# Optimization experiments

Measured on AMD Instinct MI355X. Metric: run time of the kernel, lower is better.

The kernel has to match this reference:

```python
import jax, jax.numpy as jnp
import numpy as np

B, T, C, H = 8, 512, 1024, 16
N = C // H
DW, DA, DG = 64, 64, 128  # LoRA dims for decay / icl-rate / gate at C=1024

def _ln(x, w, b, eps=1e-5):
    mu = x.mean(-1, keepdims=True)
    var = ((x - mu) ** 2).mean(-1, keepdims=True)
    return (x - mu) * jax.lax.rsqrt(var + eps) * w + b

def _gn_heads(x, w, b, eps=64e-5):
    # GroupNorm(H groups) over channel dim of (B,T,C)
    xh = x.reshape(x.shape[0], x.shape[1], H, N)
    mu = xh.mean(-1, keepdims=True)
    var = ((xh - mu) ** 2).mean(-1, keepdims=True)
    xh = (xh - mu) * jax.lax.rsqrt(var + eps)
    return xh.reshape(x.shape) * w + b

def _shift(x):
    # RWKV time_shift: ZeroPad2d((0,0,1,-1))
    return jnp.concatenate([jnp.zeros_like(x[:, :1]), x[:, :-1]], axis=1)

def _wkv7(r, w_log, k, v, a, b):
    # all (B,T,H,N); state S (B,H,N,N): S = S*diag(exp(-exp(w))) + (S@a)b^T + v k^T; out = S@r
    decay = jnp.exp(-jnp.exp(w_log))
    def step(state, inp):
        r_t, d_t, k_t, v_t, a_t, b_t = inp
        sa = jnp.einsum('bhij,bhj->bhi', state, a_t)
        state = (state * d_t[:, :, None, :]
                 + sa[..., None] * b_t[:, :, None, :]
                 + v_t[..., None] * k_t[:, :, None, :])
        return state, jnp.einsum('bhij,bhj->bhi', state, r_t)
    xs = tuple(jnp.moveaxis(t, 1, 0) for t in (r, decay, k, v, a, b))
    s0 = jnp.zeros((r.shape[0], H, N, N), r.dtype)
    _, out = jax.lax.scan(step, s0, xs)
    return jnp.moveaxis(out, 0, 1)

def reference(x, v_first, ln_pre_w, ln_pre_b, ln_attn_w, ln_attn_b, ln_ffn_w, ln_ffn_b,
              x_r, x_w, x_k, x_v, x_a, x_g, w0, w1, w2, a0, a1, a2, g1, g2,
              k_k, k_a, r_k, W_r, W_k, W_v, W_o, gn_w, gn_b,
              ffn_x_k, W_ffn1, W_ffn2):
    Bx, Tx = x.shape[0], x.shape[1]
    x = _ln(x, ln_pre_w, ln_pre_b)            # pre_norm (layer_idx==0)
    # --- time mixing (RWKV7Attention) ---
    xn = _ln(x, ln_attn_w, ln_attn_b)
    dx = _shift(xn) - xn
    xr = xn + dx * x_r; xw = xn + dx * x_w; xk = xn + dx * x_k
    xv = xn + dx * x_v; xa = xn + dx * x_a; xg = xn + dx * x_g
    r = xr @ W_r
    w_log = -jax.nn.softplus(-(w0 + jnp.tanh(xw @ w1) @ w2)) - 0.5
    k = xk @ W_k
    v = xv @ W_v
    v_first = v                               # layer 0 stores v
    a = jax.nn.sigmoid(a0 + (xa @ a1) @ a2)   # in-context learning rate
    g = jax.nn.sigmoid(xg @ g1) @ g2          # gate
    kk = (k * k_k).reshape(Bx, Tx, H, N)
    kk = kk / jnp.maximum(jnp.linalg.norm(kk, axis=-1, keepdims=True), 1e-12)
    k = k * (1.0 + (a - 1.0) * k_a)
    rh = r.reshape(Bx, Tx, H, N)
    kh = k.reshape(Bx, Tx, H, N)
    vh = v.reshape(Bx, Tx, H, N)
    ah = a.reshape(Bx, Tx, H, N)
    o = _wkv7(rh, w_log.reshape(Bx, Tx, H, N), kh, vh, -kk, kk * ah)
    o = _gn_heads(o.reshape(Bx, Tx, C), gn_w, gn_b)
    o = o + ((rh * kh * r_k).sum(-1, keepdims=True) * vh).reshape(Bx, Tx, C)
    x = x + (o * g) @ W_o                     # residual (dropout p=0)
    # --- channel mixing (RWKV7FeedForward) ---
    xf = _ln(x, ln_ffn_w, ln_ffn_b)
    kf = xf + (_shift(xf) - xf) * ffn_x_k
    x = x + jnp.square(jax.nn.relu(kf @ W_ffn1)) @ W_ffn2
    return x, v_first

def setup_inputs() -> dict:
    key = jax.random.key(0)
    ks = iter(jax.random.split(key, 40))
    def nrm(shape, s=0.02):
        return jax.random.normal(next(ks), shape, jnp.float32) * s
    f32 = jnp.float32
    d = {
        'x': jax.random.normal(next(ks), (B, T, C), f32),
        'v_first': jnp.zeros((B, T, C), f32),
        'ln_pre_w': jnp.ones((C,), f32), 'ln_pre_b': jnp.zeros((C,), f32),
        'ln_attn_w': jnp.ones((C,), f32), 'ln_attn_b': jnp.zeros((C,), f32),
        'ln_ffn_w': jnp.ones((C,), f32), 'ln_ffn_b': jnp.zeros((C,), f32),
        'x_r': nrm((C,), 0.1), 'x_w': nrm((C,), 0.1), 'x_k': nrm((C,), 0.1),
        'x_v': nrm((C,), 0.1), 'x_a': nrm((C,), 0.1), 'x_g': nrm((C,), 0.1),
        'w0': nrm((C,), 0.5), 'w1': nrm((C, DW)), 'w2': nrm((DW, C)),
        'a0': nrm((C,), 0.1), 'a1': nrm((C, DA)), 'a2': nrm((DA, C)),
        'g1': nrm((C, DG)), 'g2': nrm((DG, C)),
        'k_k': 0.85 * jnp.ones((C,), f32) + nrm((C,), 0.05),
        'k_a': jnp.ones((C,), f32),
        'r_k': nrm((H, N), 0.1),
        'W_r': nrm((C, C)), 'W_k': nrm((C, C)), 'W_v': nrm((C, C)), 'W_o': nrm((C, C)),
        'gn_w': jnp.ones((C,), f32), 'gn_b': jnp.zeros((C,), f32),
        'ffn_x_k': nrm((C,), 0.1),
        'W_ffn1': nrm((C, 4 * C)), 'W_ffn2': nrm((4 * C, C)),
    }
    return d
```

## Files before the change

### kernel.cpp

```cpp
#include <hip/hip_runtime.h>

#define Bb 8
#define Tt 512
#define Cc 1024
#define Hh 16
#define Nh 64
#define Mm 4096
#define BTC 4194304
#define DEV __device__ __forceinline__

typedef __attribute__((ext_vector_type(8))) short short8;
typedef __attribute__((ext_vector_type(4))) float f32x4;

DEV unsigned short f2bf(float f) {
  unsigned int u = __builtin_bit_cast(unsigned int, f);
  u += 0x7fffu + ((u >> 16) & 1u);
  return (unsigned short)(u >> 16);
}

template <int CTRL>
DEV float dppadd(float x) {
  int xi = __builtin_bit_cast(int, x);
  int yi = __builtin_amdgcn_update_dpp(0, xi, CTRL, 0xF, 0xF, true);
  return x + __builtin_bit_cast(float, yi);
}

struct TDesc { const float* in; unsigned short* out; int K, N, bstart, nbx; };
struct TPack { TDesc d[12]; };

__global__ __launch_bounds__(256) void kt_transpose_multi(TPack p) {
  __shared__ float tile[32][33];
  const int bid = blockIdx.x;
  int i = 0;
  #pragma unroll
  for (int j = 1; j < 12; ++j) if (bid >= p.d[j].bstart) i = j;
  const float* in = p.d[i].in;
  unsigned short* out = p.d[i].out;
  const int K = p.d[i].K, N = p.d[i].N;
  const int local = bid - p.d[i].bstart;
  const int byq = local / p.d[i].nbx;
  const int bx = (local - byq * p.d[i].nbx) * 32;
  const int by = byq * 32;
  int tx = threadIdx.x, ty = threadIdx.y;
  #pragma unroll
  for (int q = ty; q < 32; q += 8) {
    int kk = by + q, nn = bx + tx;
    tile[q][tx] = (kk < K && nn < N) ? in[(size_t)kk * N + nn] : 0.f;
  }
  __syncthreads();
  #pragma unroll
  for (int q = ty; q < 32; q += 8) {
    int nn = bx + q, kk = by + tx;
    if (nn < N && kk < K) out[(size_t)nn * K + kk] = f2bf(tile[tx][q]);
  }
}

DEV void row_stats(float v0, float v1, float v2, float v3, float* red,
                   float& mu, float& rs, float eps) {
  float s = v0 + v1 + v2 + v3;
  float q = v0 * v0 + v1 * v1 + v2 * v2 + v3 * v3;
  #pragma unroll
  for (int o = 32; o; o >>= 1) { s += __shfl_down(s, o); q += __shfl_down(q, o); }
  int w = threadIdx.x >> 6;
  __syncthreads();
  if ((threadIdx.x & 63) == 0) { red[w] = s; red[4 + w] = q; }
  __syncthreads();
  s = red[0] + red[1] + red[2] + red[3];
  q = red[4] + red[5] + red[6] + red[7];
  mu = s * (1.f / 1024.f);
  float var = q * (1.f / 1024.f) - mu * mu;
  rs = rsqrtf(var + eps);
}

__global__ __launch_bounds__(256) void k1_mix(
    const float* __restrict__ x,
    const float* __restrict__ lnpw, const float* __restrict__ lnpb,
    const float* __restrict__ lnaw, const float* __restrict__ lnab,
    const float* __restrict__ cr, const float* __restrict__ cw,
    const float* __restrict__ ck, const float* __restrict__ cv,
    const float* __restrict__ ca, const float* __restrict__ cg,
    float* __restrict__ xln,
    unsigned short* __restrict__ mR, unsigned short* __restrict__ mW,
    unsigned short* __restrict__ mK, unsigned short* __restrict__ mV,
    unsigned short* __restrict__ mA, unsigned short* __restrict__ mG) {
  __shared__ float red[8];
  const int row = blockIdx.x;
  const int t = row & (Tt - 1);
  const int tid = threadIdx.x;
  const int c = tid * 4;
  const size_t base = (size_t)row * Cc + c;
  float a0 = x[base], a1 = x[base + 1], a2 = x[base + 2], a3 = x[base + 3];
  float mu, rs;
  row_stats(a0, a1, a2, a3, red, mu, rs, 1e-5f);
  float pw0 = lnpw[c], pw1 = lnpw[c + 1], pw2 = lnpw[c + 2], pw3 = lnpw[c + 3];
  float pb0 = lnpb[c], pb1 = lnpb[c + 1], pb2 = lnpb[c + 2], pb3 = lnpb[c + 3];
  float l0 = (a0 - mu) * rs * pw0 + pb0, l1 = (a1 - mu) * rs * pw1 + pb1;
  float l2 = (a2 - mu) * rs * pw2 + pb2, l3 = (a3 - mu) * rs * pw3 + pb3;
  float4 st; st.x = l0; st.y = l1; st.z = l2; st.w = l3;
  *(float4*)(xln + base) = st;
  row_stats(l0, l1, l2, l3, red, mu, rs, 1e-5f);
  float aw0 = lnaw[c], aw1 = lnaw[c + 1], aw2 = lnaw[c + 2], aw3 = lnaw[c + 3];
  float ab0 = lnab[c], ab1 = lnab[c + 1], ab2 = lnab[c + 2], ab3 = lnab[c + 3];
  float n0 = (l0 - mu) * rs * aw0 + ab0, n1 = (l1 - mu) * rs * aw1 + ab1;
  float n2 = (l2 - mu) * rs * aw2 + ab2, n3 = (l3 - mu) * rs * aw3 + ab3;
  float p0 = 0.f, p1 = 0.f, p2 = 0.f, p3 = 0.f;
  if (t > 0) {
    const size_t pb_ = base - Cc;
    float q0 = x[pb_], q1 = x[pb_ + 1], q2 = x[pb_ + 2], q3 = x[pb_ + 3];
    row_stats(q0, q1, q2, q3, red, mu, rs, 1e-5f);
    float e0 = (q0 - mu) * rs * pw0 + pb0, e1 = (q1 - mu) * rs * pw1 + pb1;
    float e2 = (q2 - mu) * rs * pw2 + pb2, e3 = (q3 - mu) * rs * pw3 + pb3;
    row_stats(e0, e1, e2, e3, red, mu, rs, 1e-5f);
    p0 = (e0 - mu) * rs * aw0 + ab0; p1 = (e1 - mu) * rs * aw1 + ab1;
    p2 = (e2 - mu) * rs * aw2 + ab2; p3 = (e3 - mu) * rs * aw3 + ab3;
  }
  float d0 = p0 - n0, d1 = p1 - n1, d2 = p2 - n2, d3 = p3 - n3;
  #define EMIT(cf, dst) { \
    float f0 = cf[c], f1 = cf[c + 1], f2 = cf[c + 2], f3 = cf[c + 3]; \
    ushort4 u; u.x = f2bf(n0 + d0 * f0); u.y = f2bf(n1 + d1 * f1); \
    u.z = f2bf(n2 + d2 * f2); u.w = f2bf(n3 + d3 * f3); \
    *(ushort4*)(dst + base) = u; }
  EMIT(cr, mR) EMIT(cw, mW) EMIT(ck, mK) EMIT(cv, mV) EMIT(ca, mA) EMIT(cg, mG)
  #undef EMIT
}

DEV void gll16(const unsigned short* g, unsigned short* l) {
  __builtin_amdgcn_global_load_lds(
      (const __attribute__((address_space(1))) void*)g,
      (__attribute__((address_space(3))) void*)l, 16, 0, 0);
}

template <int MODE>
DEV void gemm_epi(float z, size_t oi, int col,
                  float* outF, unsigned short* outB,
                  const float* bias, const float* res, float* outF2) {
  if constexpr (MODE == 0) outF[oi] = z;
  else if constexpr (MODE == 1) outB[oi] = f2bf(z);
  else if constexpr (MODE == 2) outB[oi] = f2bf(tanhf(z));
  else if constexpr (MODE == 3) outB[oi] = f2bf(1.f / (1.f + expf(-z)));
  else if constexpr (MODE == 4) { float m = fmaxf(z, 0.f); outB[oi] = f2bf(m * m); }
  else if constexpr (MODE == 5) { z += bias[col]; outF[oi] = 1.f / (1.f + expf(-z)); }
  else if constexpr (MODE == 6) {
    z += bias[col];
    float sg = 1.f / (1.f + expf(-z));
    outF[oi] = expf(-0.6065306597126334f * sg);
  } else if constexpr (MODE == 7) { outF[oi] = z + res[oi]; }
  else { float v = z + res[oi]; outF[oi] = v; outF2[oi] = v; }
}

DEV void gemm_epi_rt(int mode, float z, size_t oi, int col,
                     float* outF, unsigned short* outB, const float* bias) {
  if (mode == 0) outF[oi] = z;
  else if (mode == 1) outB[oi] = f2bf(z);
  else if (mode == 2) outB[oi] = f2bf(tanhf(z));
  else if (mode == 3) outB[oi] = f2bf(1.f / (1.f + expf(-z)));
  else if (mode == 5) { z += bias[col]; outF[oi] = 1.f / (1.f + expf(-z)); }
  else { z += bias[col]; float sg = 1.f / (1.f + expf(-z));
         outF[oi] = expf(-0.6065306597126334f * sg); }
}

template <int MODE>
__global__ __launch_bounds__(256) void kg_gemm64(
    const unsigned short* __restrict__ A, const unsigned short* __restrict__ Bt,
    int M, int Nn, int K,
    float* __restrict__ outF, unsigned short* __restrict__ outB,
    const float* __restrict__ bias, const float* __restrict__ res,
    float* __restrict__ outF2) {
  __shared__ unsigned short lsA[128 * 32];
  __shared__ unsigned short lsB[64 * 32];
  const int tid = threadIdx.x;
  const int lane = tid & 63;
  const int wave = tid >> 6;
  const int wy = wave >> 1, wx = wave & 1;
  const int m0 = blockIdx.y * 128;
  const int n0 = blockIdx.x * 64;
  const int sl4 = lane >> 2;
  const int sc = (lane & 3) << 3;
  f32x4 acc[4][2];
  #pragma unroll
  for (int i = 0; i < 4; ++i)
    #pragma unroll
    for (int j = 0; j < 2; ++j) { f32x4 z = {0.f, 0.f, 0.f, 0.f}; acc[i][j] = z; }
  const int fr = lane & 15;
  const int fk = (lane >> 4) << 3;
  for (int k0 = 0; k0 < K; k0 += 32) {
    #pragma unroll
    for (int j = 0; j < 2; ++j) {
      const int rb = (wave + j * 4) * 16;
      gll16(A + (size_t)(m0 + rb + sl4) * K + k0 + sc, lsA + rb * 32);
    }
    {
      const int rb = wave * 16;
      int br = n0 + rb + sl4;
      br = br < Nn ? br : Nn - 1;
      gll16(Bt + (size_t)br * K + k0 + sc, lsB + rb * 32);
    }
    __syncthreads();
    short8 af[4], bf[2];
    #pragma unroll
    for (int mt = 0; mt < 4; ++mt)
      af[mt] = *(const short8*)(lsA + (wy * 64 + mt * 16 + fr) * 32 + fk);
    #pragma unroll
    for (int nt = 0; nt < 2; ++nt)
      bf[nt] = *(const short8*)(lsB + (wx * 32 + nt * 16 + fr) * 32 + fk);
    #pragma unroll
    for (int mt = 0; mt < 4; ++mt)
      #pragma unroll
      for (int nt = 0; nt < 2; ++nt)
        acc[mt][nt] = __builtin_amdgcn_mfma_f32_16x16x32_bf16(af[mt], bf[nt], acc[mt][nt], 0, 0, 0);
    __syncthreads();
  }
  const int rbase = (lane >> 4) << 2;
  const int cbase = lane & 15;
  #pragma unroll
  for (int mt = 0; mt < 4; ++mt)
    #pragma unroll
    for (int nt = 0; nt < 2; ++nt)
      #pragma unroll
      for (int rr = 0; rr < 4; ++rr) {
        int row = m0 + wy * 64 + mt * 16 + rbase + rr;
        int col = n0 + wx * 32 + nt * 16 + cbase;
        if (col < Nn)
          gemm_epi<MODE>(acc[mt][nt][rr], (size_t)row * Nn + col, col, outF, outB, bias, res, outF2);
      }
}

DEV void gemm_body_rt(const unsigned short* A, const unsigned short* Bt,
                      int Nn, int K,
                      float* outF, unsigned short* outB, const float* bias,
                      unsigned short* lsA, unsigned short* lsB,
                      int m0, int n0, int mode) {
  const int tid = threadIdx.x;
  const int lane = tid & 63;
  const int wave = tid >> 6;
  const int wy = wave >> 1, wx = wave & 1;
  const int sl4 = lane >> 2;
  const int sc = (lane & 3) << 3;
  f32x4 acc[4][2];
  #pragma unroll
  for (int i = 0; i < 4; ++i)
    #pragma unroll
    for (int j = 0; j < 2; ++j) { f32x4 z = {0.f, 0.f, 0.f, 0.f}; acc[i][j] = z; }
  const int fr = lane & 15;
  const int fk = (lane >> 4) << 3;
  for (int k0 = 0; k0 < K; k0 += 32) {
    #pragma unroll
    for (int j = 0; j < 2; ++j) {
      const int rb = (wave + j * 4) * 16;
      gll16(A + (size_t)(m0 + rb + sl4) * K + k0 + sc, lsA + rb * 32);
    }
    {
      const int rb = wave * 16;
      int br = n0 + rb + sl4;
      br = br < Nn ? br : Nn - 1;
      gll16(Bt + (size_t)br * K + k0 + sc, lsB + rb * 32);
    }
    __syncthreads();
    short8 af[4], bf[2];
    #pragma unroll
    for (int mt = 0; mt < 4; ++mt)
      af[mt] = *(const short8*)(lsA + (wy * 64 + mt * 16 + fr) * 32 + fk);
    #pragma unroll
    for (int nt = 0; nt < 2; ++nt)
      bf[nt] = *(const short8*)(lsB + (wx * 32 + nt * 16 + fr) * 32 + fk);
    #pragma unroll
    for (int mt = 0; mt < 4; ++mt)
      #pragma unroll
      for (int nt = 0; nt < 2; ++nt)
        acc[mt][nt] = __builtin_amdgcn_mfma_f32_16x16x32_bf16(af[mt], bf[nt], acc[mt][nt], 0, 0, 0);
    __syncthreads();
  }
  const int rbase = (lane >> 4) << 2;
  const int cbase = lane & 15;
  #pragma unroll
  for (int mt = 0; mt < 4; ++mt)
    #pragma unroll
    for (int nt = 0; nt < 2; ++nt)
      #pragma unroll
      for (int rr = 0; rr < 4; ++rr) {
        int row = m0 + wy * 64 + mt * 16 + rbase + rr;
        int col = n0 + wx * 32 + nt * 16 + cbase;
        if (col < Nn)
          gemm_epi_rt(mode, acc[mt][nt][rr], (size_t)row * Nn + col, col, outF, outB, bias);
      }
}

__global__ __launch_bounds__(256) void kg_lora1(
    const unsigned short* __restrict__ mW, const unsigned short* __restrict__ mA,
    const unsigned short* __restrict__ mG,
    const unsigned short* __restrict__ w1T, const unsigned short* __restrict__ a1T,
    const unsigned short* __restrict__ g1T,
    unsigned short* __restrict__ tmpw, unsigned short* __restrict__ tmpa,
    unsigned short* __restrict__ tmpg) {
  __shared__ unsigned short lsA[128 * 32];
  __shared__ unsigned short lsB[64 * 32];
  const int z = blockIdx.z;
  const unsigned short* A  = z == 0 ? mW : z == 1 ? mA : mG;
  const unsigned short* Bt = z == 0 ? w1T : z == 1 ? a1T : g1T;
  unsigned short* outB     = z == 0 ? tmpw : z == 1 ? tmpa : tmpg;
  const int Nn = z < 2 ? 64 : 128;
  const int n0 = z < 2 ? 0 : (z - 2) * 64;
  const int mode = z == 0 ? 2 : z == 1 ? 1 : 3;
  gemm_body_rt(A, Bt, Nn, 1024, nullptr, outB, nullptr, lsA, lsB,
               blockIdx.y * 128, n0, mode);
}

__global__ __launch_bounds__(256) void kg_lora2(
    const unsigned short* __restrict__ tmpw, const unsigned short* __restrict__ tmpa,
    const unsigned short* __restrict__ tmpg,
    const unsigned short* __restrict__ w2T, const unsigned short* __restrict__ a2T,
    const unsigned short* __restrict__ g2T,
    float* __restrict__ decay, float* __restrict__ aicl, float* __restrict__ gout,
    const float* __restrict__ w0v, const float* __restrict__ a0v) {
  __shared__ unsigned short lsA[128 * 32];
  __shared__ unsigned short lsB[64 * 32];
  const int z = blockIdx.z;
  const unsigned short* A  = z == 0 ? tmpw : z == 1 ? tmpa : tmpg;
  const unsigned short* Bt = z == 0 ? w2T : z == 1 ? a2T : g2T;
  float* outF              = z == 0 ? decay : z == 1 ? aicl : gout;
  const float* bias        = z == 0 ? w0v : z == 1 ? a0v : nullptr;
  const int K = z < 2 ? 64 : 128;
  const int mode = z == 0 ? 6 : z == 1 ? 5 : 0;
  gemm_body_rt(A, Bt, 1024, K, outF, nullptr, bias, lsA, lsB,
               blockIdx.y * 128, blockIdx.x * 64, mode);
}

template <int MODE>
__global__ __launch_bounds__(512, 1) void kg_gemm8p(
    const unsigned short* __restrict__ A, const unsigned short* __restrict__ Bt,
    int Nn, int Kstride, int Klen,
    float* __restrict__ outF, unsigned short* __restrict__ outB) {
  __shared__ unsigned short lds[3 * 24576];
  const int tid = threadIdx.x;
  const int lane = tid & 63;
  const int wave = tid >> 6;
  const int wm = wave >> 2, wn = wave & 3;
  const int m0 = blockIdx.y * 128;
  const int n0 = blockIdx.x * 256;
  const int kbase = blockIdx.z * Klen;
  const int ntile = Klen / 64;
  const int fr = lane & 15;
  const int fkb = (lane >> 4) << 4;

  int arow[2], acolb[2], brow[4], bcolb[4];
  #pragma unroll
  for (int i = 0; i < 2; ++i) {
    int off = i * 8192 + tid * 16;
    int r = off >> 7;
    arow[i] = r; acolb[i] = (off & 127) ^ ((r & 7) << 4);
  }
  #pragma unroll
  for (int i = 0; i < 4; ++i) {
    int off = i * 8192 + tid * 16;
    int r = off >> 7;
    brow[i] = r; bcolb[i] = (off & 127) ^ ((r & 7) << 4);
  }

  #define STAGE(t_) { \
    int tc = (t_) < ntile ? (t_) : ntile - 1; \
    unsigned short* lb_ = lds + ((t_) % 3) * 24576; \
    const int kk = kbase + tc * 64; \
    _Pragma("unroll") \
    for (int i = 0; i < 2; ++i) \
      gll16(A + (size_t)(m0 + arow[i]) * Kstride + kk + (acolb[i] >> 1), \
            lb_ + i * 4096 + wave * 512); \
    _Pragma("unroll") \
    for (int i = 0; i < 4; ++i) \
      gll16(Bt + (size_t)(n0 + brow[i]) * Kstride + kk + (bcolb[i] >> 1), \
            lb_ + 8192 + i * 4096 + wave * 512); \
  }

  f32x4 acc[4][4];
  #pragma unroll
  for (int i = 0; i < 4; ++i)
    #pragma unroll
    for (int j = 0; j < 4; ++j) { f32x4 z = {0.f, 0.f, 0.f, 0.f}; acc[i][j] = z; }

  STAGE(0)
  STAGE(1)
  asm volatile("s_waitcnt vmcnt(6)" ::: "memory");
  __syncthreads();

  for (int t = 0; t < ntile; ++t) {
    STAGE(t + 2)
    const unsigned short* lb = lds + (t % 3) * 24576;
    #pragma unroll
    for (int ks = 0; ks < 2; ++ks) {
      short8 af[4], bf[4];
      #pragma unroll
      for (int mt = 0; mt < 4; ++mt) {
        int r = wm * 64 + mt * 16 + fr;
        int byt = (ks * 64 + fkb) ^ ((r & 7) << 4);
        af[mt] = *(const short8*)(lb + r * 64 + (byt >> 1));
      }
      #pragma unroll
      for (int nt = 0; nt < 4; ++nt) {
        int r = wn * 64 + nt * 16 + fr;
        int byt = (ks * 64 + fkb) ^ ((r & 7) << 4);
        bf[nt] = *(const short8*)(lb + 8192 + r * 64 + (byt >> 1));
      }
      __builtin_amdgcn_s_setprio(1);
      #pragma unroll
      for (int mt = 0; mt < 4; ++mt)
        #pragma unroll
        for (int nt = 0; nt < 4; ++nt)
          acc[mt][nt] = __builtin_amdgcn_mfma_f32_16x16x32_bf16(af[mt], bf[nt], acc[mt][nt], 0, 0, 0);
      __builtin_amdgcn_s_setprio(0);
    }
    asm volatile("s_waitcnt vmcnt(6)" ::: "memory");
    __syncthreads();
  }
  #undef STAGE

  const int rbase = (lane >> 4) << 2;
  const int cbase = lane & 15;
  #pragma unroll
  for (int mt = 0; mt < 4; ++mt)
    #pragma unroll
    for (int nt = 0; nt < 4; ++nt)
      #pragma unroll
      for (int rr = 0; rr < 4; ++rr) {
        int row = m0 + wm * 64 + mt * 16 + rbase + rr;
        int col = n0 + wn * 64 + nt * 16 + cbase;
        size_t oi = (size_t)row * Nn + col;
        float z = acc[mt][nt][rr];
        if constexpr (MODE == 4) { float m = fmaxf(z, 0.f); outB[oi] = f2bf(m * m); }
        else atomicAdd(outF + oi, z);
      }
}

__global__ __launch_bounds__(512, 1) void kg_qkv8p(
    const unsigned short* __restrict__ A0, const unsigned short* __restrict__ A1,
    const unsigned short* __restrict__ A2,
    const unsigned short* __restrict__ B0, const unsigned short* __restrict__ B1,
    const unsigned short* __restrict__ B2,
    float* __restrict__ rbuf, float* __restrict__ kbuf, float* __restrict__ vout,
    const float* __restrict__ aicl,
    const float* __restrict__ kkc, const float* __restrict__ kac,
    float* __restrict__ awb, float* __restrict__ bwb) {
  __shared__ unsigned short lds[3 * 24576];
  const int z = blockIdx.z;
  const unsigned short* A  = z == 0 ? A0 : z == 1 ? A1 : A2;
  const unsigned short* Bt = z == 0 ? B0 : z == 1 ? B1 : B2;
  const int tid = threadIdx.x;
  const int lane = tid & 63;
  const int wave = tid >> 6;
  const int wm = wave >> 2, wn = wave & 3;
  const int m0 = blockIdx.y * 128;
  const int n0 = blockIdx.x * 256;
  const int ntile = 16;
  const int fr = lane & 15;
  const int fkb = (lane >> 4) << 4;

  int arow[2], acolb[2], brow[4], bcolb[4];
  #pragma unroll
  for (int i = 0; i < 2; ++i) {
    int off = i * 8192 + tid * 16;
    int r = off >> 7;
    arow[i] = r; acolb[i] = (off & 127) ^ ((r & 7) << 4);
  }
  #pragma unroll
  for (int i = 0; i < 4; ++i) {
    int off = i * 8192 + tid * 16;
    int r = off >> 7;
    brow[i] = r; bcolb[i] = (off & 127) ^ ((r & 7) << 4);
  }

  #define STAGE(t_) { \
    int tc = (t_) < ntile ? (t_) : ntile - 1; \
    unsigned short* lb_ = lds + ((t_) % 3) * 24576; \
    const int kk = tc * 64; \
    _Pragma("unroll") \
    for (int i = 0; i < 2; ++i) \
      gll16(A + (size_t)(m0 + arow[i]) * 1024 + kk + (acolb[i] >> 1), \
            lb_ + i * 4096 + wave * 512); \
    _Pragma("unroll") \
    for (int i = 0; i < 4; ++i) \
      gll16(Bt + (size_t)(n0 + brow[i]) * 1024 + kk + (bcolb[i] >> 1), \
            lb_ + 8192 + i * 4096 + wave * 512); \
  }

  f32x4 acc[4][4];
  #pragma unroll
  for (int i = 0; i < 4; ++i)
    #pragma unroll
    for (int j = 0; j < 4; ++j) { f32x4 zz = {0.f, 0.f, 0.f, 0.f}; acc[i][j] = zz; }

  STAGE(0)
  STAGE(1)
  asm volatile("s_waitcnt vmcnt(6)" ::: "memory");
  __syncthreads();

  for (int t = 0; t < ntile; ++t) {
    STAGE(t + 2)
    const unsigned short* lb = lds + (t % 3) * 24576;
    #pragma unroll
    for (int ks = 0; ks < 2; ++ks) {
      short8 af[4], bf[4];
      #pragma unroll
      for (int mt = 0; mt < 4; ++mt) {
        int r = wm * 64 + mt * 16 + fr;
        int byt = (ks * 64 + fkb) ^ ((r & 7) << 4);
        af[mt] = *(const short8*)(lb + r * 64 + (byt >> 1));
      }
      #pragma unroll
      for (int nt = 0; nt < 4; ++nt) {
        int r = wn * 64 + nt * 16 + fr;
        int byt = (ks * 64 + fkb) ^ ((r & 7) << 4);
        bf[nt] = *(const short8*)(lb + 8192 + r * 64 + (byt >> 1));
      }
      __builtin_amdgcn_s_setprio(1);
      #pragma unroll
      for (int mt = 0; mt < 4; ++mt)
        #pragma unroll
        for (int nt = 0; nt < 4; ++nt)
          acc[mt][nt] = __builtin_amdgcn_mfma_f32_16x16x32_bf16(af[mt], bf[nt], acc[mt][nt], 0, 0, 0);
      __builtin_amdgcn_s_setprio(0);
    }
    asm volatile("s_waitcnt vmcnt(6)" ::: "memory");
    __syncthreads();
  }
  #undef STAGE

  const int rbase = (lane >> 4) << 2;
  const int cbase = lane & 15;
  if (z != 1) {
    float* outF = z == 0 ? rbuf : vout;
    #pragma unroll
    for (int mt = 0; mt < 4; ++mt)
      #pragma unroll
      for (int nt = 0; nt < 4; ++nt)
        #pragma unroll
        for (int rr = 0; rr < 4; ++rr) {
          int row = m0 + wm * 64 + mt * 16 + rbase + rr;
          int col = n0 + wn * 64 + nt * 16 + cbase;
          outF[(size_t)row * Cc + col] = acc[mt][nt][rr];
        }
  } else {
    float kkc4[4], kac4[4];
    #pragma unroll
    for (int nt = 0; nt < 4; ++nt) {
      int col = n0 + wn * 64 + nt * 16 + cbase;
      kkc4[nt] = kkc[col];
      kac4[nt] = kac[col];
    }
    #pragma unroll
    for (int mt = 0; mt < 4; ++mt)
      #pragma unroll
      for (int rr = 0; rr < 4; ++rr) {
        int row = m0 + wm * 64 + mt * 16 + rbase + rr;
        float h0 = acc[mt][0][rr] * kkc4[0];
        float h1 = acc[mt][1][rr] * kkc4[1];
        float h2 = acc[mt][2][rr] * kkc4[2];
        float h3 = acc[mt][3][rr] * kkc4[3];
        float ss = (h0 * h0 + h1 * h1) + (h2 * h2 + h3 * h3);
        ss = dppadd<0xB1>(ss);
        ss = dppadd<0x4E>(ss);
        ss = dppadd<0x124>(ss);
        ss = dppadd<0x128>(ss);
        float inv = 1.f / fmaxf(sqrtf(ss), 1e-12f);
        #pragma unroll
        for (int nt = 0; nt < 4; ++nt) {
          int col = n0 + wn * 64 + nt * 16 + cbase;
          size_t oi = (size_t)row * Cc + col;
          float kv = acc[mt][nt][rr];
          float hn = kv * kkc4[nt] * inv;
          float av = aicl[oi];
          awb[oi] = -hn;
          bwb[oi] = hn * av;
          kbuf[oi] = kv * (1.f + (av - 1.f) * kac4[nt]);
        }
      }
  }
}

#define CS 8
__global__ __launch_bounds__(512, 2) void k5_wkv7(
    const float* __restrict__ r, const float* __restrict__ dec,
    const float* __restrict__ k, const float* __restrict__ v,
    const float* __restrict__ aw, const float* __restrict__ bw,
    float* __restrict__ o) {
  const int blk = blockIdx.x;
  const int bh = blk & 127, half = blk >> 7;
  const int b = bh >> 4, h = bh & 15;
  const int tid = threadIdx.x;
  const int lane = tid & 63;
  const int w = tid >> 6;
  const int cg = lane & 15;
  const int rw = lane >> 4;
  const int row = half * 32 + w * 4 + rw;
  const int cb = cg << 2;

  __shared__ float buf[2][6 * CS * 64];

  float S[4];
  #pragma unroll
  for (int j = 0; j < 4; ++j) S[j] = 0.f;

  const size_t base = (size_t)b * Tt * Cc + (size_t)h * Nh;

  const float* sptr = w == 0 ? aw : w == 1 ? dec : w == 2 ? bw
                    : w == 3 ? k  : w == 4 ? r   : v;
  const int srow = lane >> 4;
  const int scol = (lane & 15) << 2;

  uint4 R0, R1;
  #define LOADC(cstart) if (w < 6) { \
    const size_t g0 = base + (size_t)((cstart) + srow) * Cc + scol; \
    R0 = *(const uint4*)(sptr + g0); \
    R1 = *(const uint4*)(sptr + g0 + 4 * Cc); }

  LOADC(0)

  #pragma unroll 1
  for (int c = 0; c < Tt / CS; ++c) {
    float* bp = buf[c & 1];
    if (w < 6) {
      *(uint4*)(bp + w * 512 + (lane << 2)) = R0;
      *(uint4*)(bp + w * 512 + 256 + (lane << 2)) = R1;
    }
    const int cn = (c + 1 < Tt / CS) ? (c + 1) : c;
    LOADC(cn * CS)
    __syncthreads();

    float4 Aq[2], Dq[2], Bq[2], Kq[2], Rq[2];
    float Vv[2];
    #define LOADOPS(slot, ss) { \
      const float* sp_ = bp + (ss) * 64; \
      Aq[slot] = *(const float4*)(sp_ + cb); \
      Dq[slot] = *(const float4*)(sp_ + 512 + cb); \
      Bq[slot] = *(const float4*)(sp_ + 1024 + cb); \
      Kq[slot] = *(const float4*)(sp_ + 1536 + cb); \
      Rq[slot] = *(const float4*)(sp_ + 2048 + cb); \
      Vv[slot] = sp_[2560 + row]; }

    LOADOPS(0, 0)
    #pragma unroll
    for (int s = 0; s < CS; ++s) {
      const int cu = s & 1, nx = cu ^ 1;
      if (s + 1 < CS) LOADOPS(nx, s + 1)

      float4 a4 = Aq[cu];
      float sa = fmaf(S[1], a4.y, S[0] * a4.x) + fmaf(S[3], a4.w, S[2] * a4.z);
      sa = dppadd<0xB1>(sa);
      sa = dppadd<0x4E>(sa);
      sa = dppadd<0x124>(sa);
      sa = dppadd<0x128>(sa);

      const float vv = Vv[cu];
      float4 d4 = Dq[cu], b4 = Bq[cu], k4 = Kq[cu], r4 = Rq[cu];
      S[0] = fmaf(S[0], d4.x, fmaf(vv, k4.x, sa * b4.x));
      float oo = S[0] * r4.x;
      S[1] = fmaf(S[1], d4.y, fmaf(vv, k4.y, sa * b4.y));
      oo = fmaf(S[1], r4.y, oo);
      S[2] = fmaf(S[2], d4.z, fmaf(vv, k4.z, sa * b4.z));
      oo = fmaf(S[2], r4.z, oo);
      S[3] = fmaf(S[3], d4.w, fmaf(vv, k4.w, sa * b4.w));
      oo = fmaf(S[3], r4.w, oo);

      oo = dppadd<0xB1>(oo);
      oo = dppadd<0x4E>(oo);
      oo = dppadd<0x124>(oo);
      oo = dppadd<0x128>(oo);
      if (cg == 0) o[base + (size_t)(c * CS + s) * Cc + row] = oo;
    }
    #undef LOADOPS
  }
  #undef LOADC
}

__global__ __launch_bounds__(256) void k6_out(
    const float* __restrict__ o, const float* __restrict__ r, const float* __restrict__ k,
    const float* __restrict__ v, const float* __restrict__ rk,
    const float* __restrict__ gnw, const float* __restrict__ gnb,
    const float* __restrict__ g, unsigned short* __restrict__ og) {
  const int row = blockIdx.x, tid = threadIdx.x;
  const int c = tid * 4;
  const size_t base = (size_t)row * Cc + c;
  float o0 = o[base], o1 = o[base + 1], o2 = o[base + 2], o3 = o[base + 3];
  float r0 = r[base], r1 = r[base + 1], r2 = r[base + 2], r3 = r[base + 3];
  float k0 = k[base], k1 = k[base + 1], k2 = k[base + 2], k3 = k[base + 3];
  float s = o0 + o1 + o2 + o3;
  float q = o0 * o0 + o1 * o1 + o2 * o2 + o3 * o3;
  float bs = r0 * k0 * rk[c] + r1 * k1 * rk[c + 1] + r2 * k2 * rk[c + 2] + r3 * k3 * rk[c + 3];
  #pragma unroll
  for (int m = 8; m; m >>= 1) {
    s += __shfl_xor(s, m); q += __shfl_xor(q, m); bs += __shfl_xor(bs, m);
  }
  float mu = s * (1.f / 64.f);
  float var = q * (1.f / 64.f) - mu * mu;
  float rs = rsqrtf(var + 64e-5f);
  float v0 = v[base], v1 = v[base + 1], v2 = v[base + 2], v3 = v[base + 3];
  float z0 = (o0 - mu) * rs * gnw[c] + gnb[c] + bs * v0;
  float z1 = (o1 - mu) * rs * gnw[c + 1] + gnb[c + 1] + bs * v1;
  float z2 = (o2 - mu) * rs * gnw[c + 2] + gnb[c + 2] + bs * v2;
  float z3 = (o3 - mu) * rs * gnw[c + 3] + gnb[c + 3] + bs * v3;
  ushort4 u;
  u.x = f2bf(z0 * g[base]); u.y = f2bf(z1 * g[base + 1]);
  u.z = f2bf(z2 * g[base + 2]); u.w = f2bf(z3 * g[base + 3]);
  *(ushort4*)(og + base) = u;
}

__global__ __launch_bounds__(256) void k8_ffnmix(
    const float* __restrict__ x2, const float* __restrict__ lnw, const float* __restrict__ lnb,
    const float* __restrict__ fxk, unsigned short* __restrict__ kf) {
  __shared__ float red[8];
  const int row = blockIdx.x;
  const int t = row & (Tt - 1);
  const int tid = threadIdx.x;
  const int c = tid * 4;
  const size_t base = (size_t)row * Cc + c;
  float a0 = x2[base], a1 = x2[base + 1], a2 = x2[base + 2], a3 = x2[base + 3];
  float mu, rs;
  row_stats(a0, a1, a2, a3, red, mu, rs, 1e-5f);
  float w0 = lnw[c], w1 = lnw[c + 1], w2 = lnw[c + 2], w3 = lnw[c + 3];
  float b0 = lnb[c], b1 = lnb[c + 1], b2 = lnb[c + 2], b3 = lnb[c + 3];
  float f0 = (a0 - mu) * rs * w0 + b0, f1 = (a1 - mu) * rs * w1 + b1;
  float f2 = (a2 - mu) * rs * w2 + b2, f3 = (a3 - mu) * rs * w3 + b3;
  float p0 = 0.f, p1 = 0.f, p2 = 0.f, p3 = 0.f;
  if (t > 0) {
    const size_t pb_ = base - Cc;
    float q0 = x2[pb_], q1 = x2[pb_ + 1], q2 = x2[pb_ + 2], q3 = x2[pb_ + 3];
    row_stats(q0, q1, q2, q3, red, mu, rs, 1e-5f);
    p0 = (q0 - mu) * rs * w0 + b0; p1 = (q1 - mu) * rs * w1 + b1;
    p2 = (q2 - mu) * rs * w2 + b2; p3 = (q3 - mu) * rs * w3 + b3;
  }
  ushort4 u;
  u.x = f2bf(f0 + (p0 - f0) * fxk[c]);
  u.y = f2bf(f1 + (p1 - f1) * fxk[c + 1]);
  u.z = f2bf(f2 + (p2 - f2) * fxk[c + 2]);
  u.w = f2bf(f3 + (p3 - f3) * fxk[c + 3]);
  *(ushort4*)(kf + base) = u;
}

extern "C" void kernel_launch(void* const* d_in, const int* in_sizes, int n_in,
                              void* d_out, int out_size, void* d_ws, size_t ws_size,
                              hipStream_t stream) {
  (void)in_sizes; (void)n_in; (void)out_size; (void)ws_size;
  const float* x    = (const float*)d_in[0];
  const float* lnpw = (const float*)d_in[2];
  const float* lnpb = (const float*)d_in[3];
  const float* lnaw = (const float*)d_in[4];
  const float* lnab = (const float*)d_in[5];
  const float* lnfw = (const float*)d_in[6];
  const float* lnfb = (const float*)d_in[7];
  const float* cxr  = (const float*)d_in[8];
  const float* cxw  = (const float*)d_in[9];
  const float* cxk  = (const float*)d_in[10];
  const float* cxv  = (const float*)d_in[11];
  const float* cxa  = (const float*)d_in[12];
  const float* cxg  = (const float*)d_in[13];
  const float* w0v  = (const float*)d_in[14];
  const float* w1m  = (const float*)d_in[15];
  const float* w2m  = (const float*)d_in[16];
  const float* a0v  = (const float*)d_in[17];
  const float* a1m  = (const float*)d_in[18];
  const float* a2m  = (const float*)d_in[19];
  const float* g1m  = (const float*)d_in[20];
  const float* g2m  = (const float*)d_in[21];
  const float* kkv  = (const float*)d_in[22];
  const float* kav  = (const float*)d_in[23];
  const float* rkv  = (const float*)d_in[24];
  const float* Wr   = (const float*)d_in[25];
  const float* Wk   = (const float*)d_in[26];
  const float* Wv   = (const float*)d_in[27];
  const float* Wo   = (const float*)d_in[28];
  const float* gnw  = (const float*)d_in[29];
  const float* gnb  = (const float*)d_in[30];
  const float* fxk  = (const float*)d_in[31];
  const float* Wf1  = (const float*)d_in[32];
  const float* Wf2  = (const float*)d_in[33];

  char* ws = (char*)d_ws;
  float* outx = (float*)d_out;
  float* vout = outx + BTC;

  size_t off = 0;
  unsigned short* WrT  = (unsigned short*)(ws + off); off += 2097152;
  unsigned short* WkT  = (unsigned short*)(ws + off); off += 2097152;
  unsigned short* WvT  = (unsigned short*)(ws + off); off += 2097152;
  unsigned short* WoT  = (unsigned short*)(ws + off); off += 2097152;
  unsigned short* Wf1T = (unsigned short*)(ws + off); off += 8388608;
  unsigned short* Wf2T = (unsigned short*)(ws + off); off += 8388608;
  unsigned short* w1T  = (unsigned short*)(ws + off); off += 131072;
  unsigned short* w2T  = (unsigned short*)(ws + off); off += 131072;
  unsigned short* a1T  = (unsigned short*)(ws + off); off += 131072;
  unsigned short* a2T  = (unsigned short*)(ws + off); off += 131072;
  unsigned short* g1T  = (unsigned short*)(ws + off); off += 262144;
  unsigned short* g2T  = (unsigned short*)(ws + off); off += 262144;
  float* xln = (float*)(ws + off); off += 16777216;
  unsigned short* mixR = (unsigned short*)(ws + off);
  unsigned short* mixW = (unsigned short*)(ws + off + 8388608);
  unsigned short* mixK = (unsigned short*)(ws + off + 16777216);
  unsigned short* mixV = (unsigned short*)(ws + off + 25165824);
  unsigned short* mixA = (unsigned short*)(ws + off + 33554432);
  unsigned short* mixG = (unsigned short*)(ws + off + 41943040);
  unsigned short* hbuf = (unsigned short*)(ws + off);
  off += 50331648;
  unsigned short* tmpw = (unsigned short*)(ws + off); off += 524288;
  unsigned short* tmpa = (unsigned short*)(ws + off); off += 524288;
  unsigned short* tmpg = (unsigned short*)(ws + off); off += 1048576;
  float* decay = (float*)(ws + off);
  unsigned short* og = (unsigned short*)(ws + off);
  off += 16777216;
  float* aicl = (float*)(ws + off);
  float* obuf = (float*)(ws + off);
  off += 16777216;
  float* gout = (float*)(ws + off); off += 16777216;
  float* rbuf = (float*)(ws + off);
  float* x2   = (float*)(ws + off);
  off += 16777216;
  float* kbuf = (float*)(ws + off); off += 16777216;
  float* awb  = (float*)(ws + off);
  unsigned short* kf = (unsigned short*)(ws + off);
  off += 16777216;
  float* bwb  = (float*)(ws + off); off += 16777216;

  dim3 tb(32, 8);
  TPack tp;
  tp.d[0]  = TDesc{Wr,  WrT,  1024, 1024, 0,     32};
  tp.d[1]  = TDesc{Wk,  WkT,  1024, 1024, 1024,  32};
  tp.d[2]  = TDesc{Wv,  WvT,  1024, 1024, 2048,  32};
  tp.d[3]  = TDesc{Wo,  WoT,  1024, 1024, 3072,  32};
  tp.d[4]  = TDesc{Wf1, Wf1T, 1024, 4096, 4096,  128};
  tp.d[5]  = TDesc{Wf2, Wf2T, 4096, 1024, 8192,  32};
  tp.d[6]  = TDesc{w1m, w1T,  1024, 64,   12288, 2};
  tp.d[7]  = TDesc{w2m, w2T,  64,   1024, 12352, 32};
  tp.d[8]  = TDesc{a1m, a1T,  1024, 64,   12416, 2};
  tp.d[9]  = TDesc{a2m, a2T,  64,   1024, 12480, 32};
  tp.d[10] = TDesc{g1m, g1T,  1024, 128,  12544, 4};
  tp.d[11] = TDesc{g2m, g2T,  128,  1024, 12672, 32};
  kt_transpose_multi<<<12800, tb, 0, stream>>>(tp);

  k1_mix<<<Mm, 256, 0, stream>>>(x, lnpw, lnpb, lnaw, lnab, cxr, cxw, cxk, cxv, cxa, cxg,
                                 xln, mixR, mixW, mixK, mixV, mixA, mixG);

  kg_lora1<<<dim3(1, 32, 4), 256, 0, stream>>>(mixW, mixA, mixG, w1T, a1T, g1T,
                                               tmpw, tmpa, tmpg);
  kg_lora2<<<dim3(16, 32, 3), 256, 0, stream>>>(tmpw, tmpa, tmpg, w2T, a2T, g2T,
                                                decay, aicl, gout, w0v, a0v);

  kg_qkv8p<<<dim3(4, 32, 3), 512, 0, stream>>>(mixR, mixK, mixV, WrT, WkT, WvT,
                                               rbuf, kbuf, vout,
                                               aicl, kkv, kav, awb, bwb);

  k5_wkv7<<<256, 512, 0, stream>>>(rbuf, decay, kbuf, vout, awb, bwb, obuf);
  k6_out<<<Mm, 256, 0, stream>>>(obuf, rbuf, kbuf, vout, rkv, gnw, gnb, gout, og);
  kg_gemm64<9><<<dim3(16, 32), 256, 0, stream>>>(og, WoT, Mm, 1024, 1024, x2, nullptr, nullptr, xln, outx);
  k8_ffnmix<<<Mm, 256, 0, stream>>>(x2, lnfw, lnfb, fxk, kf);
  kg_gemm8p<4><<<dim3(16, 32, 1), 512, 0, stream>>>(kf, Wf1T, 4096, 1024, 1024, nullptr, hbuf);
  kg_gemm8p<8><<<dim3(4, 32, 2), 512, 0, stream>>>(hbuf, Wf2T, 1024, 4096, 2048, outx, nullptr);
}
```

Before: 556.4 us.

## Use 64-row GEMM tiles for QKV and FFN2, drop split-K atomics

The QKV projection kernel moves from 128x256 to 64x256 output tiles, which doubles the block count for better CU occupancy and shrinks the LDS footprint. The FFN down-projection no longer uses a 2-way split-K with atomicAdd into a buffer pre-seeded by the Wo GEMM. It instead uses a new 64-row tile kernel over the full K that adds the residual x2 in its epilogue. The Wo GEMM therefore no longer writes a duplicate copy of its output, which removes the extra store and the atomic traffic. The cost is lower arithmetic intensity per tile and a longer K loop per block for FFN2.

After: 558.3 us. No clear change (+0.3%).

```diff
diff --git a/kernel.cpp b/kernel.cpp
--- a/kernel.cpp
+++ b/kernel.cpp
@@ -133,7 +133,7 @@
 template <int MODE>
 DEV void gemm_epi(float z, size_t oi, int col,
                   float* outF, unsigned short* outB,
-                  const float* bias, const float* res, float* outF2) {
+                  const float* bias, const float* res) {
   if constexpr (MODE == 0) outF[oi] = z;
   else if constexpr (MODE == 1) outB[oi] = f2bf(z);
   else if constexpr (MODE == 2) outB[oi] = f2bf(tanhf(z));
@@ -144,8 +144,7 @@
     z += bias[col];
     float sg = 1.f / (1.f + expf(-z));
     outF[oi] = expf(-0.6065306597126334f * sg);
-  } else if constexpr (MODE == 7) { outF[oi] = z + res[oi]; }
-  else { float v = z + res[oi]; outF[oi] = v; outF2[oi] = v; }
+  } else { outF[oi] = z + res[oi]; }
 }
 
 DEV void gemm_epi_rt(int mode, float z, size_t oi, int col,
@@ -164,8 +163,7 @@
     const unsigned short* __restrict__ A, const unsigned short* __restrict__ Bt,
     int M, int Nn, int K,
     float* __restrict__ outF, unsigned short* __restrict__ outB,
-    const float* __restrict__ bias, const float* __restrict__ res,
-    float* __restrict__ outF2) {
+    const float* __restrict__ bias, const float* __restrict__ res) {
   __shared__ unsigned short lsA[128 * 32];
   __shared__ unsigned short lsB[64 * 32];
   const int tid = threadIdx.x;
@@ -221,7 +219,7 @@
         int row = m0 + wy * 64 + mt * 16 + rbase + rr;
         int col = n0 + wx * 32 + nt * 16 + cbase;
         if (col < Nn)
-          gemm_epi<MODE>(acc[mt][nt][rr], (size_t)row * Nn + col, col, outF, outB, bias, res, outF2);
+          gemm_epi<MODE>(acc[mt][nt][rr], (size_t)row * Nn + col, col, outF, outB, bias, res);
       }
 }
 
@@ -425,11 +423,112 @@
         size_t oi = (size_t)row * Nn + col;
         float z = acc[mt][nt][rr];
         if constexpr (MODE == 4) { float m = fmaxf(z, 0.f); outB[oi] = f2bf(m * m); }
-        else atomicAdd(outF + oi, z);
-      }
-}
-
-__global__ __launch_bounds__(512, 1) void kg_qkv8p(
+        else outF[oi] = z;
+      }
+}
+
+template <int MODE>
+__global__ __launch_bounds__(512, 1) void kg_gemm8p64(
+    const unsigned short* __restrict__ A, const unsigned short* __restrict__ Bt,
+    int Nn, int Kstride, int Klen,
+    float* __restrict__ outF, unsigned short* __restrict__ outB,
+    const float* __restrict__ res) {
+  __shared__ unsigned short lds[3 * 20480];
+  const int tid = threadIdx.x;
+  const int lane = tid & 63;
+  const int wave = tid >> 6;
+  const int wm = wave >> 2, wn = wave & 3;
+  const int m0 = blockIdx.y * 64;
+  const int n0 = blockIdx.x * 256;
+  const int ntile = Klen / 64;
+  const int fr = lane & 15;
+  const int fkb = (lane >> 4) << 4;
+
+  int arow, acolb, brow[4], bcolb[4];
+  {
+    int off = tid * 16;
+    int r = off >> 7;
+    arow = r; acolb = (off & 127) ^ ((r & 7) << 4);
+  }
+  #pragma unroll
+  for (int i = 0; i < 4; ++i) {
+    int off = i * 8192 + tid * 16;
+    int r = off >> 7;
+    brow[i] = r; bcolb[i] = (off & 127) ^ ((r & 7) << 4);
+  }
+
+  #define STAGE(t_) { \
+    int tc = (t_) < ntile ? (t_) : ntile - 1; \
+    unsigned short* lb_ = lds + ((t_) % 3) * 20480; \
+    const int kk = tc * 64; \
+    gll16(A + (size_t)(m0 + arow) * Kstride + kk + (acolb >> 1), \
+          lb_ + wave * 512); \
+    _Pragma("unroll") \
+    for (int i = 0; i < 4; ++i) \
+      gll16(Bt + (size_t)(n0 + brow[i]) * Kstride + kk + (bcolb[i] >> 1), \
+            lb_ + 4096 + i * 4096 + wave * 512); \
+  }
+
+  f32x4 acc[2][4];
+  #pragma unroll
+  for (int i = 0; i < 2; ++i)
+    #pragma unroll
+    for (int j = 0; j < 4; ++j) { f32x4 z = {0.f, 0.f, 0.f, 0.f}; acc[i][j] = z; }
+
+  STAGE(0)
+  STAGE(1)
+  asm volatile("s_waitcnt vmcnt(5)" ::: "memory");
+  __syncthreads();
+
+  for (int t = 0; t < ntile; ++t) {
+    STAGE(t + 2)
+    const unsigned short* lb = lds + (t % 3) * 20480;
+    #pragma unroll
+    for (int ks = 0; ks < 2; ++ks) {
+      short8 af[2], bf[4];
+      #pragma unroll
+      for (int mt = 0; mt < 2; ++mt) {
+        int r = wm * 32 + mt * 16 + fr;
+        int byt = (ks * 64 + fkb) ^ ((r & 7) << 4);
+        af[mt] = *(const short8*)(lb + r * 64 + (byt >> 1));
+      }
+      #pragma unroll
+      for (int nt = 0; nt < 4; ++nt) {
+        int r = wn * 64 + nt * 16 + fr;
+        int byt = (ks * 64 + fkb) ^ ((r & 7) << 4);
+        bf[nt] = *(const short8*)(lb + 4096 + r * 64 + (byt >> 1));
+      }
+      __builtin_amdgcn_s_setprio(1);
+      #pragma unroll
+      for (int mt = 0; mt < 2; ++mt)
+        #pragma unroll
+        for (int nt = 0; nt < 4; ++nt)
+          acc[mt][nt] = __builtin_amdgcn_mfma_f32_16x16x32_bf16(af[mt], bf[nt], acc[mt][nt], 0, 0, 0);
+      __builtin_amdgcn_s_setprio(0);
+    }
+    asm volatile("s_waitcnt vmcnt(5)" ::: "memory");
+    __syncthreads();
+  }
+  #undef STAGE
+
+  const int rbase = (lane >> 4) << 2;
+  const int cbase = lane & 15;
+  #pragma unroll
+  for (int mt = 0; mt < 2; ++mt)
+    #pragma unroll
+    for (int nt = 0; nt < 4; ++nt)
+      #pragma unroll
+      for (int rr = 0; rr < 4; ++rr) {
+        int row = m0 + wm * 32 + mt * 16 + rbase + rr;
+        int col = n0 + wn * 64 + nt * 16 + cbase;
+        size_t oi = (size_t)row * Nn + col;
+        float z = acc[mt][nt][rr];
+        if constexpr (MODE == 7) outF[oi] = z + res[oi];
+        else outF[oi] = z;
+      }
+}
+
+__global__ __launch_bounds__(512, 1) void kg_qkv8p64(
     const unsigned short* __restrict__ A0, const unsigned short* __restrict__ A1,
     const unsigned short* __restrict__ A2,
     const unsigned short* __restrict__ B0, const unsigned short* __restrict__ B1,
@@ -438,7 +537,7 @@
     const float* __restrict__ aicl,
     const float* __restrict__ kkc, const float* __restrict__ kac,
     float* __restrict__ awb, float* __restrict__ bwb) {
-  __shared__ unsigned short lds[3 * 24576];
+  __shared__ unsigned short lds[3 * 20480];
   const int z = blockIdx.z;
   const unsigned short* A  = z == 0 ? A0 : z == 1 ? A1 : A2;
   const unsigned short* Bt = z == 0 ? B0 : z == 1 ? B1 : B2;
@@ -446,18 +545,17 @@
   const int lane = tid & 63;
   const int wave = tid >> 6;
   const int wm = wave >> 2, wn = wave & 3;
-  const int m0 = blockIdx.y * 128;
+  const int m0 = blockIdx.y * 64;
   const int n0 = blockIdx.x * 256;
   const int ntile = 16;
   const int fr = lane & 15;
   const int fkb = (lane >> 4) << 4;
 
-  int arow[2], acolb[2], brow[4], bcolb[4];
-  #pragma unroll
-  for (int i = 0; i < 2; ++i) {
-    int off = i * 8192 + tid * 16;
+  int arow, acolb, brow[4], bcolb[4];
+  {
+    int off = tid * 16;
     int r = off >> 7;
-    arow[i] = r; acolb[i] = (off & 127) ^ ((r & 7) << 4);
+    arow = r; acolb = (off & 127) ^ ((r & 7) << 4);
   }
   #pragma unroll
   for (int i = 0; i < 4; ++i) {
@@ -468,38 +566,36 @@
 
   #define STAGE(t_) { \
     int tc = (t_) < ntile ? (t_) : ntile - 1; \
-    unsigned short* lb_ = lds + ((t_) % 3) * 24576; \
+    unsigned short* lb_ = lds + ((t_) % 3) * 20480; \
     const int kk = tc * 64; \
-    _Pragma("unroll") \
-    for (int i = 0; i < 2; ++i) \
-      gll16(A + (size_t)(m0 + arow[i]) * 1024 + kk + (acolb[i] >> 1), \
-            lb_ + i * 4096 + wave * 512); \
+    gll16(A + (size_t)(m0 + arow) * 1024 + kk + (acolb >> 1), \
+          lb_ + wave * 512); \
     _Pragma("unroll") \
     for (int i = 0; i < 4; ++i) \
       gll16(Bt + (size_t)(n0 + brow[i]) * 1024 + kk + (bcolb[i] >> 1), \
-            lb_ + 8192 + i * 4096 + wave * 512); \
-  }
-
-  f32x4 acc[4][4];
-  #pragma unroll
-  for (int i = 0; i < 4; ++i)
+            lb_ + 4096 + i * 4096 + wave * 512); \
+  }
+
+  f32x4 acc[2][4];
+  #pragma unroll
+  for (int i = 0; i < 2; ++i)
     #pragma unroll
     for (int j = 0; j < 4; ++j) { f32x4 zz = {0.f, 0.f, 0.f, 0.f}; acc[i][j] = zz; }
 
   STAGE(0)
   STAGE(1)
-  asm volatile("s_waitcnt vmcnt(6)" ::: "memory");
+  asm volatile("s_waitcnt vmcnt(5)" ::: "memory");
   __syncthreads();
 
   for (int t = 0; t < ntile; ++t) {
     STAGE(t + 2)
-    const unsigned short* lb = lds + (t % 3) * 24576;
+    const unsigned short* lb = lds + (t % 3) * 20480;
     #pragma unroll
     for (int ks = 0; ks < 2; ++ks) {
-      short8 af[4], bf[4];
-      #pragma unroll
-      for (int mt = 0; mt < 4; ++mt) {
-        int r = wm * 64 + mt * 16 + fr;
+      short8 af[2], bf[4];
+      #pragma unroll
+      for (int mt = 0; mt < 2; ++mt) {
+        int r = wm * 32 + mt * 16 + fr;
         int byt = (ks * 64 + fkb) ^ ((r & 7) << 4);
         af[mt] = *(const short8*)(lb + r * 64 + (byt >> 1));
       }
@@ -507,17 +603,17 @@
       for (int nt = 0; nt < 4; ++nt) {
         int r = wn * 64 + nt * 16 + fr;
         int byt = (ks * 64 + fkb) ^ ((r & 7) << 4);
-        bf[nt] = *(const short8*)(lb + 8192 + r * 64 + (byt >> 1));
+        bf[nt] = *(const short8*)(lb + 4096 + r * 64 + (byt >> 1));
       }
       __builtin_amdgcn_s_setprio(1);
       #pragma unroll
-      for (int mt = 0; mt < 4; ++mt)
+      for (int mt = 0; mt < 2; ++mt)
         #pragma unroll
         for (int nt = 0; nt < 4; ++nt)
           acc[mt][nt] = __builtin_amdgcn_mfma_f32_16x16x32_bf16(af[mt], bf[nt], acc[mt][nt], 0, 0, 0);
       __builtin_amdgcn_s_setprio(0);
     }
-    asm volatile("s_waitcnt vmcnt(6)" ::: "memory");
+    asm volatile("s_waitcnt vmcnt(5)" ::: "memory");
     __syncthreads();
   }
   #undef STAGE
@@ -527,12 +623,12 @@
   if (z != 1) {
     float* outF = z == 0 ? rbuf : vout;
     #pragma unroll
-    for (int mt = 0; mt < 4; ++mt)
+    for (int mt = 0; mt < 2; ++mt)
       #pragma unroll
       for (int nt = 0; nt < 4; ++nt)
         #pragma unroll
         for (int rr = 0; rr < 4; ++rr) {
-          int row = m0 + wm * 64 + mt * 16 + rbase + rr;
+          int row = m0 + wm * 32 + mt * 16 + rbase + rr;
           int col = n0 + wn * 64 + nt * 16 + cbase;
           outF[(size_t)row * Cc + col] = acc[mt][nt][rr];
         }
@@ -545,10 +641,10 @@
       kac4[nt] = kac[col];
     }
     #pragma unroll
-    for (int mt = 0; mt < 4; ++mt)
+    for (int mt = 0; mt < 2; ++mt)
       #pragma unroll
       for (int rr = 0; rr < 4; ++rr) {
-        int row = m0 + wm * 64 + mt * 16 + rbase + rr;
+        int row = m0 + wm * 32 + mt * 16 + rbase + rr;
         float h0 = acc[mt][0][rr] * kkc4[0];
         float h1 = acc[mt][1][rr] * kkc4[1];
         float h2 = acc[mt][2][rr] * kkc4[2];
@@ -840,14 +936,14 @@
   kg_lora2<<<dim3(16, 32, 3), 256, 0, stream>>>(tmpw, tmpa, tmpg, w2T, a2T, g2T,
                                                 decay, aicl, gout, w0v, a0v);
 
-  kg_qkv8p<<<dim3(4, 32, 3), 512, 0, stream>>>(mixR, mixK, mixV, WrT, WkT, WvT,
-                                               rbuf, kbuf, vout,
-                                               aicl, kkv, kav, awb, bwb);
+  kg_qkv8p64<<<dim3(4, 64, 3), 512, 0, stream>>>(mixR, mixK, mixV, WrT, WkT, WvT,
+                                                 rbuf, kbuf, vout,
+                                                 aicl, kkv, kav, awb, bwb);
 
   k5_wkv7<<<256, 512, 0, stream>>>(rbuf, decay, kbuf, vout, awb, bwb, obuf);
   k6_out<<<Mm, 256, 0, stream>>>(obuf, rbuf, kbuf, vout, rkv, gnw, gnb, gout, og);
-  kg_gemm64<9><<<dim3(16, 32), 256, 0, stream>>>(og, WoT, Mm, 1024, 1024, x2, nullptr, nullptr, xln, outx);
+  kg_gemm64<7><<<dim3(16, 32), 256, 0, stream>>>(og, WoT, Mm, 1024, 1024, x2, nullptr, nullptr, xln);
   k8_ffnmix<<<Mm, 256, 0, stream>>>(x2, lnfw, lnfb, fxk, kf);
   kg_gemm8p<4><<<dim3(16, 32, 1), 512, 0, stream>>>(kf, Wf1T, 4096, 1024, 1024, nullptr, hbuf);
-  kg_gemm8p<8><<<dim3(4, 32, 2), 512, 0, stream>>>(hbuf, Wf2T, 1024, 4096, 2048, outx, nullptr);
-}
+  kg_gemm8p64<7><<<dim3(4, 64), 512, 0, stream>>>(hbuf, Wf2T, 1024, 4096, 4096, outx, nullptr, x2);
+}
```
